# Kernel tuning notes

Measured on AMD Instinct MI355X. Metric: run time of the kernel, lower is better.

## Reference

```python
import jax, jax.numpy as jnp
import numpy as np

NEG_SLOPE = 0.2


def setup_inputs() -> dict:
    key = jax.random.key(0)
    k1, k2, k3 = jax.random.split(key, 3)
    B, N, IN, OUT, C = 2048, 256, 256, 256, 1024
    x = jax.random.normal(k1, (B, N, IN), dtype=jnp.float32)
    indices = jax.random.randint(k2, (B,), 0, C)
    # kaiming-uniform-like init for weight
    bound = float(np.sqrt(6.0 / IN))
    weight = jax.random.uniform(k3, (C, IN, OUT), dtype=jnp.float32, minval=-bound, maxval=bound)
    bias = jnp.zeros((1, 1, OUT), dtype=jnp.float32)
    return {"x": x, "indices": indices, "weight": weight, "bias": bias}


def reference(x, indices, weight, bias):
    # gather per-batch weight tiles: [B, IN, OUT], then batched matmul
    w = weight[indices]                      # [B, IN, OUT]
    out = jnp.einsum('bni,bio->bno', x, w)   # [B, N, OUT]
    out = out + bias[0]                      # bias[0] is [1, OUT], broadcasts
    return jnp.where(out >= 0, out, NEG_SLOPE * out)  # LeakyReLU(0.2)
```

## Files before the change

### kernel.cpp

```cpp
#include <hip/hip_runtime.h>
#include <hip/hip_bf16.h>


#define N_DIM 256
#define K_DIM 256
#define O_DIM 256
#define BK 32

typedef __attribute__((ext_vector_type(8))) __bf16 bf16x8;
typedef __attribute__((ext_vector_type(4))) float f32x4;
typedef __attribute__((ext_vector_type(4))) unsigned int u32x4;

__device__ __forceinline__ f32x4 MFMA(u32x4 a, u32x4 b, f32x4 c) {
    return __builtin_amdgcn_mfma_f32_16x16x32_bf16(
        __builtin_bit_cast(bf16x8, a), __builtin_bit_cast(bf16x8, b), c, 0, 0, 0);
}

__device__ __forceinline__ unsigned pk2(float a, float b) {
    __hip_bfloat16 ha = __float2bfloat16(a);
    __hip_bfloat16 hb = __float2bfloat16(b);
    unsigned short sa, sb;
    __builtin_memcpy(&sa, &ha, 2);
    __builtin_memcpy(&sb, &hb, 2);
    return (unsigned)sa | ((unsigned)sb << 16);
}

__global__ __launch_bounds__(256) void argemm_kernel(
    const float* __restrict__ x,
    const int* __restrict__ idx,
    const float* __restrict__ w,
    const float* __restrict__ bias,
    float* __restrict__ out)
{
    __shared__ __align__(16) char lds[65536];

    const int tid = threadIdx.x;
    const int l   = tid & 63;
    const int wid = tid >> 6;
    const int wr  = wid >> 1;
    const int wc  = wid & 1;

    const unsigned bid     = blockIdx.x;
    const unsigned chunk   = gridDim.x >> 3;
    const unsigned logical = (bid & 7u) * chunk + (bid >> 3);
    const int b    = (int)(logical >> 2);
    const int tpos = (int)(logical & 3u);
    const int n0   = (tpos >> 1) * 128;
    const int o0   = (tpos & 1) * 128;

    const int c = idx[b];
    const float* xb = x + (size_t)b * (N_DIM * K_DIM);
    const float* wb = w + (size_t)c * (K_DIM * O_DIM);

    char* A_lds = lds;
    char* B_lds = lds + 32768;

    int gA[4], gB[4];
    {
        const int lr3 = l >> 3;
        const int clA = (l & 7) ^ lr3;
#pragma unroll
        for (int q = 0; q < 4; ++q) {
            const int rA = wid * 32 + q * 8 + lr3;
            gA[q] = (n0 + rA) * K_DIM + clA * 4;
            const int kB  = wid * 8 + q * 2 + (l >> 5);
            const int clB = (l & 31) ^ (((kB >> 3) & 1) << 2);
            gB[q] = kB * O_DIM + o0 + clB * 4;
        }
    }

    auto stage = [&](int t, int buf) {
        char* Ad = A_lds + buf * 16384 + wid * 4096;
        char* Bd = B_lds + buf * 16384 + wid * 4096;
#pragma unroll
        for (int q = 0; q < 4; ++q) {
            __builtin_amdgcn_global_load_lds(
                (const __attribute__((address_space(1))) void*)(xb + gA[q] + t * BK),
                (__attribute__((address_space(3))) void*)(Ad + q * 1024), 16, 0, 0);
            __builtin_amdgcn_global_load_lds(
                (const __attribute__((address_space(1))) void*)(wb + gB[q] + t * (BK * O_DIM)),
                (__attribute__((address_space(3))) void*)(Bd + q * 1024), 16, 0, 0);
        }
    };

    f32x4 acc[4][4];
#pragma unroll
    for (int m = 0; m < 4; ++m)
#pragma unroll
        for (int n = 0; n < 4; ++n)
            acc[m][n] = (f32x4){0.f, 0.f, 0.f, 0.f};

    const int g = l >> 4;
    const int i = l & 15;

    stage(0, 0);

#pragma unroll
    for (int t = 0; t < 8; ++t) {
        const int cur = t & 1;

        if (t < 7) {
            stage(t + 1, cur ^ 1);
            asm volatile("s_waitcnt vmcnt(8)" ::: "memory");
        } else {
            asm volatile("s_waitcnt vmcnt(0)" ::: "memory");
        }
        __builtin_amdgcn_s_barrier();

        const char* Ab = A_lds + cur * 16384;
        const char* Bb = B_lds + cur * 16384;

        u32x4 af[4];
#pragma unroll
        for (int m = 0; m < 4; ++m) {
            const int row = wr * 64 + m * 16 + i;
            const int sw  = (row & 7) << 4;
            const f32x4 lo = *(const f32x4*)(Ab + row * 128 + ((g * 32) ^ sw));
            const f32x4 hi = *(const f32x4*)(Ab + row * 128 + ((g * 32 + 16) ^ sw));
            u32x4 a;
            a.x = pk2(lo.x, lo.y); a.y = pk2(lo.z, lo.w);
            a.z = pk2(hi.x, hi.y); a.w = pk2(hi.z, hi.w);
            af[m] = a;
        }

        const int ph = (g & 1) << 6;
#pragma unroll
        for (int n = 0; n < 4; ++n) {
            const int col = wc * 64 + n * 16 + i;
            const int cb  = (col * 4) ^ ph;
            float f[8];
#pragma unroll
            for (int j = 0; j < 8; ++j)
                f[j] = *(const float*)(Bb + (g * 8 + j) * 512 + cb);
            u32x4 bq;
            bq.x = pk2(f[0], f[1]); bq.y = pk2(f[2], f[3]);
            bq.z = pk2(f[4], f[5]); bq.w = pk2(f[6], f[7]);
#pragma unroll
            for (int m = 0; m < 4; ++m)
                acc[m][n] = MFMA(af[m], bq, acc[m][n]);
        }

        asm volatile("s_waitcnt lgkmcnt(0)" ::: "memory");
        __builtin_amdgcn_sched_barrier(0);
        __builtin_amdgcn_s_barrier();
    }

    float biasf[4];
#pragma unroll
    for (int n = 0; n < 4; ++n)
        biasf[n] = bias[o0 + wc * 64 + n * 16 + i];

    float* ob = out + (size_t)b * (N_DIM * O_DIM);
#pragma unroll
    for (int m = 0; m < 4; ++m) {
#pragma unroll
        for (int r = 0; r < 4; ++r) {
            const int row = n0 + wr * 64 + m * 16 + g * 4 + r;
#pragma unroll
            for (int n = 0; n < 4; ++n) {
                float v = acc[m][n][r] + biasf[n];
                v = (v >= 0.f) ? v : 0.2f * v;
                ob[row * O_DIM + o0 + wc * 64 + n * 16 + i] = v;
            }
        }
    }
}

extern "C" void kernel_launch(void* const* d_in, const int* in_sizes, int n_in,
                              void* d_out, int out_size, void* d_ws, size_t ws_size,
                              hipStream_t stream) {
    const float* x    = (const float*)d_in[0];
    const int*   idx  = (const int*)d_in[1];
    const float* w    = (const float*)d_in[2];
    const float* bias = (const float*)d_in[3];
    float*       out  = (float*)d_out;
    (void)d_ws; (void)ws_size; (void)n_in; (void)out_size;

    const int B = in_sizes[1];
    dim3 grid((unsigned)(B * 4)), block(256);
    hipLaunchKernelGGL(argemm_kernel, grid, block, 0, stream, x, idx, w, bias, out);
}
```

Measured before the change: 307.6 us.

## Convert tiles to bf16 in registers before LDS store with swizzled K-major layout

Replaces direct global-to-LDS fp32 staging with register loads that are converted to bf16 and packed before being written to LDS. B is transposed to a K-contiguous layout, so MFMA operands become single 16-byte LDS reads instead of many scalar reads plus per-iteration conversion. This halves LDS footprint and traffic and removes redundant conversions across waves. It adds a register-prefetch pipeline two tiles ahead and relies on compiler-inserted vmcnt waits, which may expose global load latency.

```diff
diff --git a/kernel.cpp b/kernel.cpp
--- a/kernel.cpp
+++ b/kernel.cpp
@@ -10,6 +10,7 @@
 typedef __attribute__((ext_vector_type(8))) __bf16 bf16x8;
 typedef __attribute__((ext_vector_type(4))) float f32x4;
 typedef __attribute__((ext_vector_type(4))) unsigned int u32x4;
+typedef __attribute__((ext_vector_type(2))) unsigned int u32x2;
 
 __device__ __forceinline__ f32x4 MFMA(u32x4 a, u32x4 b, f32x4 c) {
     return __builtin_amdgcn_mfma_f32_16x16x32_bf16(
@@ -25,6 +26,12 @@
     return (unsigned)sa | ((unsigned)sb << 16);
 }
 
+__device__ __forceinline__ int swz(int row, int k) {
+    const int rp = row >> 1;
+    const int ch = (((row & 1) << 2) + (k >> 3)) ^ (rp & 7);
+    return rp * 128 + ch * 16 + (k & 7) * 2;
+}
+
 __global__ __launch_bounds__(256) void argemm_kernel(
     const float* __restrict__ x,
     const int* __restrict__ idx,
@@ -32,7 +39,7 @@
     const float* __restrict__ bias,
     float* __restrict__ out)
 {
-    __shared__ __align__(16) char lds[65536];
+    __shared__ __align__(16) char lds[32768];
 
     const int tid = threadIdx.x;
     const int l   = tid & 63;
@@ -52,34 +59,57 @@
     const float* xb = x + (size_t)b * (N_DIM * K_DIM);
     const float* wb = w + (size_t)c * (K_DIM * O_DIM);
 
-    char* A_lds = lds;
-    char* B_lds = lds + 32768;
+    const int lr3 = l >> 3, kc = l & 7;
+    int gA[4], aW[4];
+#pragma unroll
+    for (int q = 0; q < 4; ++q) {
+        const int rA = wid * 32 + q * 8 + lr3;
+        gA[q] = (n0 + rA) * K_DIM + kc * 4;
+        aW[q] = swz(rA, kc * 4);
+    }
+    const int kq = tid >> 5;
+    const int m4 = (tid & 31) * 4;
+    int gB[4], bW[4];
+#pragma unroll
+    for (int dk = 0; dk < 4; ++dk)
+        gB[dk] = (kq * 4 + dk) * O_DIM + o0 + m4;
+#pragma unroll
+    for (int j = 0; j < 4; ++j)
+        bW[j] = 16384 + swz(m4 + j, kq * 4);
 
-    int gA[4], gB[4];
-    {
-        const int lr3 = l >> 3;
-        const int clA = (l & 7) ^ lr3;
+    const int g = l >> 4;
+    const int i = l & 15;
+    int aR[4], bR[4];
+#pragma unroll
+    for (int m = 0; m < 4; ++m) aR[m] = swz(wr * 64 + m * 16 + i, g * 8);
+#pragma unroll
+    for (int n = 0; n < 4; ++n) bR[n] = 16384 + swz(wc * 64 + n * 16 + i, g * 8);
+
+    f32x4 ra[4], rb[4];
+
+    auto issue = [&](int t) {
+#pragma unroll
+        for (int q = 0; q < 4; ++q)
+            ra[q] = *(const f32x4*)(xb + gA[q] + t * BK);
+#pragma unroll
+        for (int dk = 0; dk < 4; ++dk)
+            rb[dk] = *(const f32x4*)(wb + gB[dk] + t * (BK * O_DIM));
+    };
+    auto flush = [&](int buf) {
+        char* base = (char*)lds + buf * 8192;
 #pragma unroll
         for (int q = 0; q < 4; ++q) {
-            const int rA = wid * 32 + q * 8 + lr3;
-            gA[q] = (n0 + rA) * K_DIM + clA * 4;
-            const int kB  = wid * 8 + q * 2 + (l >> 5);
-            const int clB = (l & 31) ^ (((kB >> 3) & 1) << 2);
-            gB[q] = kB * O_DIM + o0 + clB * 4;
+            u32x2 p;
+            p.x = pk2(ra[q].x, ra[q].y);
+            p.y = pk2(ra[q].z, ra[q].w);
+            *(u32x2*)(base + aW[q]) = p;
         }
-    }
-
-    auto stage = [&](int t, int buf) {
-        char* Ad = A_lds + buf * 16384 + wid * 4096;
-        char* Bd = B_lds + buf * 16384 + wid * 4096;
 #pragma unroll
-        for (int q = 0; q < 4; ++q) {
-            __builtin_amdgcn_global_load_lds(
-                (const __attribute__((address_space(1))) void*)(xb + gA[q] + t * BK),
-                (__attribute__((address_space(3))) void*)(Ad + q * 1024), 16, 0, 0);
-            __builtin_amdgcn_global_load_lds(
-                (const __attribute__((address_space(1))) void*)(wb + gB[q] + t * (BK * O_DIM)),
-                (__attribute__((address_space(3))) void*)(Bd + q * 1024), 16, 0, 0);
+        for (int j = 0; j < 4; ++j) {
+            u32x2 p;
+            p.x = pk2(rb[0][j], rb[1][j]);
+            p.y = pk2(rb[2][j], rb[3][j]);
+            *(u32x2*)(base + bW[j]) = p;
         }
     };
 
@@ -90,59 +120,37 @@
         for (int n = 0; n < 4; ++n)
             acc[m][n] = (f32x4){0.f, 0.f, 0.f, 0.f};
 
-    const int g = l >> 4;
-    const int i = l & 15;
-
-    stage(0, 0);
+    issue(0);
+    flush(0);
+    issue(1);
+    asm volatile("s_waitcnt lgkmcnt(0)" ::: "memory");
+    __builtin_amdgcn_sched_barrier(0);
+    __builtin_amdgcn_s_barrier();
 
 #pragma unroll
     for (int t = 0; t < 8; ++t) {
         const int cur = t & 1;
-
-        if (t < 7) {
-            stage(t + 1, cur ^ 1);
-            asm volatile("s_waitcnt vmcnt(8)" ::: "memory");
-        } else {
-            asm volatile("s_waitcnt vmcnt(0)" ::: "memory");
-        }
-        __builtin_amdgcn_s_barrier();
-
-        const char* Ab = A_lds + cur * 16384;
-        const char* Bb = B_lds + cur * 16384;
+        const char* base = (const char*)lds + cur * 8192;
 
         u32x4 af[4];
 #pragma unroll
-        for (int m = 0; m < 4; ++m) {
-            const int row = wr * 64 + m * 16 + i;
-            const int sw  = (row & 7) << 4;
-            const f32x4 lo = *(const f32x4*)(Ab + row * 128 + ((g * 32) ^ sw));
-            const f32x4 hi = *(const f32x4*)(Ab + row * 128 + ((g * 32 + 16) ^ sw));
-            u32x4 a;
-            a.x = pk2(lo.x, lo.y); a.y = pk2(lo.z, lo.w);
-            a.z = pk2(hi.x, hi.y); a.w = pk2(hi.z, hi.w);
-            af[m] = a;
-        }
-
-        const int ph = (g & 1) << 6;
+        for (int m = 0; m < 4; ++m)
+            af[m] = *(const u32x4*)(base + aR[m]);
 #pragma unroll
         for (int n = 0; n < 4; ++n) {
-            const int col = wc * 64 + n * 16 + i;
-            const int cb  = (col * 4) ^ ph;
-            float f[8];
-#pragma unroll
-            for (int j = 0; j < 8; ++j)
-                f[j] = *(const float*)(Bb + (g * 8 + j) * 512 + cb);
-            u32x4 bq;
-            bq.x = pk2(f[0], f[1]); bq.y = pk2(f[2], f[3]);
-            bq.z = pk2(f[4], f[5]); bq.w = pk2(f[6], f[7]);
+            const u32x4 bq = *(const u32x4*)(base + bR[n]);
 #pragma unroll
             for (int m = 0; m < 4; ++m)
                 acc[m][n] = MFMA(af[m], bq, acc[m][n]);
         }
 
-        asm volatile("s_waitcnt lgkmcnt(0)" ::: "memory");
-        __builtin_amdgcn_sched_barrier(0);
-        __builtin_amdgcn_s_barrier();
+        if (t < 7) {
+            flush(cur ^ 1);
+            if (t < 6) issue(t + 2);
+            asm volatile("s_waitcnt lgkmcnt(0)" ::: "memory");
+            __builtin_amdgcn_sched_barrier(0);
+            __builtin_amdgcn_s_barrier();
+        }
     }
 
     float biasf[4];
```

New measurement: 307.7 us. No clear change (+0.0%).
